# Performance work log

Hardware: AMD Instinct MI355X
Metric: run time of the kernel (lower is better)

## Reference

```python
import jax, jax.numpy as jnp
import numpy as np

N = 250_000          # number of 3D points (CSR groups)
F_PROJ = 32          # projection feature dim
F_MOD = 128          # modality feature dim
NUM_GROUPS = 4       # attention groups (divides F_MOD)
IN0 = F_PROJ * 3 + 1 # in_proj*(1+proj_min+proj_max)+proj_num = 97
EPS_SM = 1e-12       # softmax eps (from segment_csr_softmax)
EPS_BN = 1e-5        # BatchNorm1d eps


def setup_inputs() -> dict:
    rng = np.random.default_rng(0)
    sizes = rng.integers(1, 8, size=N)                 # views per point in [1,7]
    csr_idx = np.concatenate([[0], np.cumsum(sizes)]).astype(np.int64)
    V = int(csr_idx[-1])                               # total mapped elements (~1M)
    ks = jax.random.split(jax.random.key(0), 6)
    return {
        "x_mod": jax.random.normal(ks[0], (V, F_MOD), jnp.float32),
        "x_proj": jax.random.normal(ks[1], (V, F_PROJ), jnp.float32),
        "csr_idx": jnp.asarray(csr_idx),
        # MLP_proj: Linear(97,4) -> BN(4) -> ReLU
        "W1": jax.random.normal(ks[2], (IN0, 4), jnp.float32) * (1.0 / np.sqrt(IN0)),
        "b1": jnp.zeros((4,), jnp.float32),
        "bn_gamma": jnp.ones((4,), jnp.float32),
        "bn_beta": jnp.zeros((4,), jnp.float32),
        # MLP_score: Linear(4, num_groups) (in_proj_3 = 4 <= 16 branch)
        "Ws": jax.random.normal(ks[3], (4, NUM_GROUPS), jnp.float32) * 0.5,
        "bs": jnp.zeros((NUM_GROUPS,), jnp.float32),
        # Gating params
        "gate_w": jnp.ones((1, NUM_GROUPS), jnp.float32),
        "gate_b": jnp.zeros((1, NUM_GROUPS), jnp.float32),
    }


def reference(x_mod, x_proj, csr_idx, W1, b1, bn_gamma, bn_beta, Ws, bs, gate_w, gate_b):
    n = csr_idx.shape[0] - 1
    V = x_mod.shape[0]
    sizes = csr_idx[1:] - csr_idx[:-1]                       # [N] group sizes
    seg = jnp.repeat(jnp.arange(n), sizes, total_repeat_length=V)  # dense group id per element

    # --- projection feature augmentation (proj_min, proj_max, proj_num) ---
    mn = jax.ops.segment_min(x_proj, seg, num_segments=n)
    mx = jax.ops.segment_max(x_proj, seg, num_segments=n)
    sizes_f = sizes.astype(jnp.float32)
    p_num = jnp.sqrt(1.0 / sizes_f)[seg][:, None]            # [V,1]
    feats = jnp.concatenate([x_proj, x_proj - mn[seg], x_proj - mx[seg], p_num], axis=1)  # [V,97]

    # --- MLP_proj: Linear -> BatchNorm1d (training-mode batch stats) -> ReLU ---
    h = feats @ W1 + b1                                      # [V,4]
    mean = h.mean(axis=0)
    var = h.var(axis=0)                                      # biased, as torch BN normalization
    h = jax.nn.relu((h - mean) * jax.lax.rsqrt(var + EPS_BN) * bn_gamma + bn_beta)

    # --- MLP_score (use_mod=False): single Linear ---
    C = h @ Ws + bs                                          # [V,G]

    # --- scaled segment CSR softmax ---
    cmax = jax.ops.segment_max(C, seg, num_segments=n)       # [N,G]
    centered = (C - cmax[seg]) / jnp.sqrt(sizes_f)[seg][:, None]  # group_scaling=True
    e = jnp.exp(centered)
    denom = jax.ops.segment_sum(e, seg, num_segments=n) + EPS_SM
    A = e / denom[seg]                                       # [V,G]

    # --- weighted pooling; expand_group_feat = uniform channel repeat (128/4=32) ---
    rep = F_MOD // NUM_GROUPS
    x_pool = jax.ops.segment_sum(x_mod * jnp.repeat(A, rep, axis=1), seg, num_segments=n)  # [N,F_MOD]

    # --- gating on per-group max score ---
    G = jnp.tanh(jax.nn.relu(gate_w * cmax + gate_b))        # [N,G]
    x_pool = x_pool * jnp.repeat(G, rep, axis=1)

    x_seen = sizes > 0                                       # [N] bool
    return x_pool, x_seen
```

## Files before the change

kernel.cpp:

```cpp
#include <hip/hip_runtime.h>


#define K1A_BLOCK 256
#define K1B_BLOCK 256
#define K3_BLOCK 256
#define K1B_MAXBLOCKS 2048

__device__ inline float4 bfly32_sum(float4 p) {
#pragma unroll
    for (int m = 16; m >= 1; m >>= 1) {
        p.x += __shfl_xor(p.x, m, 32);
        p.y += __shfl_xor(p.y, m, 32);
        p.z += __shfl_xor(p.z, m, 32);
        p.w += __shfl_xor(p.w, m, 32);
    }
    return p;
}

__global__ __launch_bounds__(K1A_BLOCK) void k1a_base(
    const float* __restrict__ xp, const int* __restrict__ csr,
    const float* __restrict__ W1, const float* __restrict__ b1,
    float* __restrict__ hbuf, int N)
{
    const int lane32 = threadIdx.x & 31;
    const int halfIdx = threadIdx.x >> 5;
    const int halves = K1A_BLOCK >> 5;
    const int gstride = gridDim.x * halves;
    const int d = lane32;
    const float4 wb = *(const float4*)(W1 + (32 + d) * 4);
    const float4 wc = *(const float4*)(W1 + (64 + d) * 4);
    const float4 w96 = *(const float4*)(W1 + 96 * 4);
    const float4 b1v = *(const float4*)(b1);

    for (int g = blockIdx.x * halves + halfIdx; g < N; g += gstride) {
        const int r0 = csr[g];
        const int size = csr[g + 1] - r0;
        const float pnum = rsqrtf((float)size);

        float mn = 1e30f, mx = -1e30f;
#pragma unroll
        for (int j = 0; j < 8; ++j) {
            if (j < size) {
                const float x = xp[(size_t)(r0 + j) * 32 + d];
                mn = fminf(mn, x);
                mx = fmaxf(mx, x);
            }
        }

        float4 pb = make_float4(-(mn * wb.x + mx * wc.x), -(mn * wb.y + mx * wc.y),
                                -(mn * wb.z + mx * wc.z), -(mn * wb.w + mx * wc.w));
        pb = bfly32_sum(pb);

        const int c = lane32 & 3;
        const float basec = (c == 0) ? pb.x + b1v.x + pnum * w96.x
                          : (c == 1) ? pb.y + b1v.y + pnum * w96.y
                          : (c == 2) ? pb.z + b1v.z + pnum * w96.z
                                     : pb.w + b1v.w + pnum * w96.w;
        if (lane32 < 4 * size) hbuf[(size_t)4 * r0 + lane32] = basec;
    }
}

__global__ __launch_bounds__(K1B_BLOCK) void k1b_mat(
    const float* __restrict__ xp, const float* __restrict__ W1,
    float* __restrict__ hbuf, float* __restrict__ partials, int V)
{
    const int tid = threadIdx.x;
    const int c = tid & 3;
    float wcol[32];
#pragma unroll
    for (int d = 0; d < 32; ++d)
        wcol[d] = W1[d * 4 + c] + W1[(32 + d) * 4 + c] + W1[(64 + d) * 4 + c];

    const int slot = (blockIdx.x * K1B_BLOCK + tid) >> 2;
    const int nslots = (gridDim.x * K1B_BLOCK) >> 2;
    float s = 0.f, ss = 0.f;
    for (int v = slot; v < V; v += nslots) {
        const float* row = xp + (size_t)v * 32;
        float acc = hbuf[(size_t)4 * v + c];
#pragma unroll
        for (int d = 0; d < 32; d += 4) {
            const float4 x4 = *(const float4*)(row + d);
            acc += x4.x * wcol[d] + x4.y * wcol[d + 1]
                 + x4.z * wcol[d + 2] + x4.w * wcol[d + 3];
        }
        hbuf[(size_t)4 * v + c] = acc;
        s += acc;
        ss += acc * acc;
    }

    __shared__ float rs[K1B_BLOCK], rss[K1B_BLOCK];
    rs[tid] = s; rss[tid] = ss;
    __syncthreads();
#pragma unroll
    for (int off = K1B_BLOCK / 2; off >= 4; off >>= 1) {
        if (tid < off) { rs[tid] += rs[tid + off]; rss[tid] += rss[tid + off]; }
        __syncthreads();
    }
    if (tid < 4) {
        partials[blockIdx.x * 8 + tid] = rs[tid];
        partials[blockIdx.x * 8 + 4 + tid] = rss[tid];
    }
}

__global__ void k2_bnfold(const float* __restrict__ partials, int nb,
                          const float* __restrict__ gamma,
                          const float* __restrict__ beta,
                          float* __restrict__ scsh, float invV)
{
    __shared__ float red[256];
    const int tid = threadIdx.x;
    const int c = tid & 7;
    float s = 0.f;
    for (int b = tid >> 3; b < nb; b += 32) s += partials[b * 8 + c];
    red[tid] = s;
    __syncthreads();
    for (int off = 128; off >= 8; off >>= 1) {
        if (tid < off) red[tid] += red[tid + off];
        __syncthreads();
    }
    if (tid < 4) {
        const float mean = red[tid] * invV;
        float var = red[4 + tid] * invV - mean * mean;
        var = fmaxf(var, 0.f);
        const float sc = gamma[tid] * rsqrtf(var + 1e-5f);
        scsh[tid] = sc;
        scsh[4 + tid] = beta[tid] - mean * sc;
    }
}

__global__ __launch_bounds__(K3_BLOCK) void k3_pool(
    const float* __restrict__ xmod, const float* __restrict__ hbuf,
    const int* __restrict__ csr, const float* __restrict__ Ws,
    const float* __restrict__ bs, const float* __restrict__ gw,
    const float* __restrict__ gb, const float* __restrict__ scsh,
    float* __restrict__ outp, float* __restrict__ outseen, int N)
{
    const int lane = threadIdx.x & 63;
    const int waveIdx = threadIdx.x >> 6;
    const int wavesPerBlock = blockDim.x >> 6;
    const int gstride = gridDim.x * wavesPerBlock;
    int g = blockIdx.x * wavesPerBlock + waveIdx;

    const int gi = lane >> 4;
    const float ws0 = Ws[0 * 4 + gi], ws1 = Ws[1 * 4 + gi];
    const float ws2 = Ws[2 * 4 + gi], ws3 = Ws[3 * 4 + gi];
    const float bsv = bs[gi];
    const float gwv = gw[gi], gbv = gb[gi];
    const float4 sc = *(const float4*)(scsh);
    const float4 sh = *(const float4*)(scsh + 4);

    for (; g < N; g += gstride) {
        const int r0 = csr[g];
        const int size = csr[g + 1] - r0;
        const float rs = rsqrtf((float)size);

        float cj[8];
        float cmax = -1e30f;
#pragma unroll
        for (int j = 0; j < 8; ++j) {
            if (j < size) {
                const float4 hv = *(const float4*)(hbuf + (size_t)(r0 + j) * 4);
                const float v0 = fmaxf(hv.x * sc.x + sh.x, 0.f);
                const float v1 = fmaxf(hv.y * sc.y + sh.y, 0.f);
                const float v2 = fmaxf(hv.z * sc.z + sh.z, 0.f);
                const float v3 = fmaxf(hv.w * sc.w + sh.w, 0.f);
                const float c = v0 * ws0 + v1 * ws1 + v2 * ws2 + v3 * ws3 + bsv;
                cj[j] = c;
                cmax = fmaxf(cmax, c);
            }
        }

        float denom = 1e-12f;
#pragma unroll
        for (int j = 0; j < 8; ++j) {
            if (j < size) {
                cj[j] = expf((cj[j] - cmax) * rs);
                denom += cj[j];
            }
        }
        const float inv = 1.0f / denom;
        const float G = tanhf(fmaxf(gwv * cmax + gbv, 0.f));

        float2 acc = make_float2(0.f, 0.f);
#pragma unroll
        for (int j = 0; j < 8; ++j) {
            if (j < size) {
                const float2 xm = *(const float2*)(xmod + (size_t)(r0 + j) * 128 + 2 * lane);
                const float a = cj[j] * inv;
                acc.x += xm.x * a;
                acc.y += xm.y * a;
            }
        }
        *(float2*)(outp + (size_t)g * 128 + 2 * lane) = make_float2(acc.x * G, acc.y * G);
        if (lane == 0) outseen[g] = (size > 0) ? 1.0f : 0.0f;
    }
}

extern "C" void kernel_launch(void* const* d_in, const int* in_sizes, int n_in,
                              void* d_out, int out_size, void* d_ws, size_t ws_size,
                              hipStream_t stream) {
    const float* xmod  = (const float*)d_in[0];
    const float* xproj = (const float*)d_in[1];
    const int*   csr   = (const int*)d_in[2];
    const float* W1    = (const float*)d_in[3];
    const float* b1    = (const float*)d_in[4];
    const float* gamma = (const float*)d_in[5];
    const float* beta  = (const float*)d_in[6];
    const float* Ws    = (const float*)d_in[7];
    const float* bs    = (const float*)d_in[8];
    const float* gw    = (const float*)d_in[9];
    const float* gb    = (const float*)d_in[10];

    const int V = in_sizes[0] / 128;
    const int N = in_sizes[2] - 1;

    float* outp = (float*)d_out;
    float* outseen = outp + (size_t)N * 128;

    float* hbuf = (float*)d_ws;
    float* partials = hbuf + (size_t)V * 4;
    float* scsh = partials + (size_t)K1B_MAXBLOCKS * 8;

    const int halves1 = K1A_BLOCK / 32;
    int blocks1a = (N + halves1 - 1) / halves1;
    if (blocks1a > 4096) blocks1a = 4096;
    k1a_base<<<blocks1a, K1A_BLOCK, 0, stream>>>(xproj, csr, W1, b1, hbuf, N);

    const int elemsPerBlock = K1B_BLOCK / 4;
    int blocks1b = (V + elemsPerBlock - 1) / elemsPerBlock;
    if (blocks1b > K1B_MAXBLOCKS) blocks1b = K1B_MAXBLOCKS;
    k1b_mat<<<blocks1b, K1B_BLOCK, 0, stream>>>(xproj, W1, hbuf, partials, V);

    k2_bnfold<<<1, 256, 0, stream>>>(partials, blocks1b, gamma, beta, scsh,
                                     1.0f / (float)V);

    const int wavesPerBlock3 = K3_BLOCK / 64;
    int blocks3 = (N + wavesPerBlock3 - 1) / wavesPerBlock3;
    if (blocks3 > 8192) blocks3 = 8192;
    k3_pool<<<blocks3, K3_BLOCK, 0, stream>>>(xmod, hbuf, csr, Ws, bs, gw, gb, scsh,
                                              outp, outseen, N);
}
```

Before: 922.0 us.

## Split attention scoring into separate kernel and pool two groups per wave

Softmax scores, group normalisation and the gate are now computed in a new kernel, one 32-lane half-wave per group, with each lane handling one element/group pair. The results are written as pre-scaled attention weights to a workspace buffer. The pooling kernel then reads those weights and handles two CSR groups per wave with non-persistent grids, so the heavy x_mod streaming loop carries less redundant scalar and transcendental work and has more loads in flight. The cost is an extra launch plus an extra V×4 write and read of the weight buffer.

```diff
diff --git a/kernel.cpp b/kernel.cpp
--- a/kernel.cpp
+++ b/kernel.cpp
@@ -3,7 +3,6 @@
 
 #define K1A_BLOCK 256
 #define K1B_BLOCK 256
-#define K3_BLOCK 256
 #define K1B_MAXBLOCKS 2048
 
 __device__ inline float4 bfly32_sum(float4 p) {
@@ -128,72 +127,105 @@
     }
 }
 
-__global__ __launch_bounds__(K3_BLOCK) void k3_pool(
-    const float* __restrict__ xmod, const float* __restrict__ hbuf,
-    const int* __restrict__ csr, const float* __restrict__ Ws,
-    const float* __restrict__ bs, const float* __restrict__ gw,
-    const float* __restrict__ gb, const float* __restrict__ scsh,
-    float* __restrict__ outp, float* __restrict__ outseen, int N)
-{
-    const int lane = threadIdx.x & 63;
-    const int waveIdx = threadIdx.x >> 6;
-    const int wavesPerBlock = blockDim.x >> 6;
-    const int gstride = gridDim.x * wavesPerBlock;
-    int g = blockIdx.x * wavesPerBlock + waveIdx;
-
-    const int gi = lane >> 4;
-    const float ws0 = Ws[0 * 4 + gi], ws1 = Ws[1 * 4 + gi];
-    const float ws2 = Ws[2 * 4 + gi], ws3 = Ws[3 * 4 + gi];
-    const float bsv = bs[gi];
-    const float gwv = gw[gi], gbv = gb[gi];
+__global__ __launch_bounds__(256) void k2b_attn(
+    const float* __restrict__ hbuf, const int* __restrict__ csr,
+    const float* __restrict__ Ws, const float* __restrict__ bs,
+    const float* __restrict__ gw, const float* __restrict__ gb,
+    const float* __restrict__ scsh, float* __restrict__ aprime,
+    float* __restrict__ outseen, int N)
+{
+    const int lane32 = threadIdx.x & 31;
+    const int g = blockIdx.x * 8 + (threadIdx.x >> 5);
+    if (g >= N) return;
+    const int c = lane32 & 3;
+    const int jmine = lane32 >> 2;
+
     const float4 sc = *(const float4*)(scsh);
     const float4 sh = *(const float4*)(scsh + 4);
-
-    for (; g < N; g += gstride) {
-        const int r0 = csr[g];
-        const int size = csr[g + 1] - r0;
-        const float rs = rsqrtf((float)size);
-
-        float cj[8];
-        float cmax = -1e30f;
-#pragma unroll
-        for (int j = 0; j < 8; ++j) {
-            if (j < size) {
-                const float4 hv = *(const float4*)(hbuf + (size_t)(r0 + j) * 4);
-                const float v0 = fmaxf(hv.x * sc.x + sh.x, 0.f);
-                const float v1 = fmaxf(hv.y * sc.y + sh.y, 0.f);
-                const float v2 = fmaxf(hv.z * sc.z + sh.z, 0.f);
-                const float v3 = fmaxf(hv.w * sc.w + sh.w, 0.f);
-                const float c = v0 * ws0 + v1 * ws1 + v2 * ws2 + v3 * ws3 + bsv;
-                cj[j] = c;
-                cmax = fmaxf(cmax, c);
-            }
-        }
-
-        float denom = 1e-12f;
-#pragma unroll
-        for (int j = 0; j < 8; ++j) {
-            if (j < size) {
-                cj[j] = expf((cj[j] - cmax) * rs);
-                denom += cj[j];
-            }
-        }
-        const float inv = 1.0f / denom;
-        const float G = tanhf(fmaxf(gwv * cmax + gbv, 0.f));
-
-        float2 acc = make_float2(0.f, 0.f);
-#pragma unroll
-        for (int j = 0; j < 8; ++j) {
-            if (j < size) {
-                const float2 xm = *(const float2*)(xmod + (size_t)(r0 + j) * 128 + 2 * lane);
-                const float a = cj[j] * inv;
-                acc.x += xm.x * a;
-                acc.y += xm.y * a;
-            }
-        }
-        *(float2*)(outp + (size_t)g * 128 + 2 * lane) = make_float2(acc.x * G, acc.y * G);
-        if (lane == 0) outseen[g] = (size > 0) ? 1.0f : 0.0f;
-    }
+    const float wc0 = Ws[0 * 4 + c], wc1 = Ws[1 * 4 + c];
+    const float wc2 = Ws[2 * 4 + c], wc3 = Ws[3 * 4 + c];
+    const float bsc = bs[c], gwc = gw[c], gbc = gb[c];
+
+    const int r0 = csr[g];
+    const int size = csr[g + 1] - r0;
+    const float rs = rsqrtf((float)size);
+
+    float cj[8];
+    float cmax = -1e30f;
+#pragma unroll
+    for (int j = 0; j < 8; ++j) {
+        if (j < size) {
+            const float4 hv = *(const float4*)(hbuf + (size_t)4 * (r0 + j));
+            const float v0 = fmaxf(hv.x * sc.x + sh.x, 0.f);
+            const float v1 = fmaxf(hv.y * sc.y + sh.y, 0.f);
+            const float v2 = fmaxf(hv.z * sc.z + sh.z, 0.f);
+            const float v3 = fmaxf(hv.w * sc.w + sh.w, 0.f);
+            cj[j] = v0 * wc0 + v1 * wc1 + v2 * wc2 + v3 * wc3 + bsc;
+            cmax = fmaxf(cmax, cj[j]);
+        }
+    }
+    float denom = 1e-12f;
+#pragma unroll
+    for (int j = 0; j < 8; ++j) {
+        if (j < size) {
+            cj[j] = expf((cj[j] - cmax) * rs);
+            denom += cj[j];
+        }
+    }
+    const float G = tanhf(fmaxf(gwc * cmax + gbc, 0.f));
+    const float scale = G / denom;
+
+    float aj = 0.f;
+#pragma unroll
+    for (int j = 0; j < 8; ++j)
+        if (j == jmine) aj = cj[j];
+    if (lane32 < 4 * size) aprime[(size_t)4 * r0 + lane32] = aj * scale;
+    if (lane32 == 0) outseen[g] = (size > 0) ? 1.0f : 0.0f;
+}
+
+__global__ __launch_bounds__(256) void k3_pool(
+    const float* __restrict__ xmod, const float* __restrict__ aprime,
+    const int* __restrict__ csr, float* __restrict__ outp, int N)
+{
+    const int lane = threadIdx.x & 63;
+    const int waveId = blockIdx.x * 4 + (threadIdx.x >> 6);
+    const int g0 = waveId * 2;
+    const int g1 = g0 + 1;
+    if (g0 >= N) return;
+    const int gi = lane >> 4;
+    const bool hasb = (g1 < N);
+
+    const int r0a = csr[g0];
+    const int sza = csr[g0 + 1] - r0a;
+    int r0b = 0, szb = 0;
+    if (hasb) { r0b = csr[g1]; szb = csr[g1 + 1] - r0b; }
+
+    float aa[8], ab[8];
+#pragma unroll
+    for (int j = 0; j < 8; ++j) {
+        aa[j] = (j < sza) ? aprime[(size_t)4 * (r0a + j) + gi] : 0.f;
+        ab[j] = (hasb && j < szb) ? aprime[(size_t)4 * (r0b + j) + gi] : 0.f;
+    }
+
+    float2 acca = make_float2(0.f, 0.f), accb = make_float2(0.f, 0.f);
+#pragma unroll
+    for (int j = 0; j < 8; ++j) {
+        if (j < sza) {
+            const float2 x = *(const float2*)(xmod + (size_t)(r0a + j) * 128 + 2 * lane);
+            acca.x += x.x * aa[j];
+            acca.y += x.y * aa[j];
+        }
+    }
+#pragma unroll
+    for (int j = 0; j < 8; ++j) {
+        if (hasb && j < szb) {
+            const float2 x = *(const float2*)(xmod + (size_t)(r0b + j) * 128 + 2 * lane);
+            accb.x += x.x * ab[j];
+            accb.y += x.y * ab[j];
+        }
+    }
+    *(float2*)(outp + (size_t)g0 * 128 + 2 * lane) = acca;
+    if (hasb) *(float2*)(outp + (size_t)g1 * 128 + 2 * lane) = accb;
 }
 
 extern "C" void kernel_launch(void* const* d_in, const int* in_sizes, int n_in,
@@ -220,6 +252,7 @@
     float* hbuf = (float*)d_ws;
     float* partials = hbuf + (size_t)V * 4;
     float* scsh = partials + (size_t)K1B_MAXBLOCKS * 8;
+    float* aprime = scsh + 8;
 
     const int halves1 = K1A_BLOCK / 32;
     int blocks1a = (N + halves1 - 1) / halves1;
@@ -234,9 +267,10 @@
     k2_bnfold<<<1, 256, 0, stream>>>(partials, blocks1b, gamma, beta, scsh,
                                      1.0f / (float)V);
 
-    const int wavesPerBlock3 = K3_BLOCK / 64;
-    int blocks3 = (N + wavesPerBlock3 - 1) / wavesPerBlock3;
-    if (blocks3 > 8192) blocks3 = 8192;
-    k3_pool<<<blocks3, K3_BLOCK, 0, stream>>>(xmod, hbuf, csr, Ws, bs, gw, gb, scsh,
-                                              outp, outseen, N);
-}
+    int blocks2b = (N + 7) / 8;
+    k2b_attn<<<blocks2b, 256, 0, stream>>>(hbuf, csr, Ws, bs, gw, gb, scsh,
+                                           aprime, outseen, N);
+
+    int blocks3 = (N + 7) / 8;
+    k3_pool<<<blocks3, 256, 0, stream>>>(xmod, aprime, csr, outp, N);
+}
```

After: 926.4 us. About the same (+0.5%).
